# Kernel optimization log

Hardware: AMD Instinct MI355X
Metric: run time of the kernel (lower is better)

The kernel has to match this reference:

```python
import jax, jax.numpy as jnp
import numpy as np

NOISE_EPS = 0.01
TOP_K = 2


def setup_inputs() -> dict:
    key = jax.random.key(0)
    k1, k2, k3, k4 = jax.random.split(key, 4)
    B, S, D, E = 8, 4096, 1024, 16
    x = jax.random.normal(k1, (B, S, D), dtype=jnp.float32)
    noise = jax.random.normal(k2, (B * S, E), dtype=jnp.float32)
    # xavier_uniform for Linear(D, E): bound = sqrt(6/(D+E))
    bound = float(np.sqrt(6.0 / (D + E)))
    W_gate = jax.random.uniform(k3, (E, D), dtype=jnp.float32, minval=-bound, maxval=bound)
    W_noise = jax.random.uniform(k4, (E, D), dtype=jnp.float32, minval=-bound, maxval=bound)
    return {"x": x, "noise": noise, "W_gate": W_gate, "W_noise": W_noise}


def reference(x, noise, W_gate, W_noise):
    # flatten tokens: (B,S,D) -> (N,D)
    orig_shape = x.shape
    x_flat = x.reshape(-1, x.shape[-1])
    clean_logits = jnp.einsum('nd,ed->ne', x_flat, W_gate)          # (N, E)
    noise_logits = jnp.einsum('nd,ed->ne', x_flat, W_noise)         # (N, E)
    noisy_logits = clean_logits + noise * jax.nn.softplus(noise_logits) * NOISE_EPS
    gates = jax.nn.softmax(noisy_logits, axis=-1)                   # (N, E)
    top_k_gates, top_k_indices = jax.lax.top_k(gates, TOP_K)        # (N, k)
    top_k_gates = top_k_gates / (jnp.sum(top_k_gates, axis=-1, keepdims=True) + 1e-8)
    load = jnp.sum(gates, axis=0)                                    # (E,)
    new_shape = orig_shape[:-1] + (TOP_K,)
    top_k_gates = top_k_gates.reshape(new_shape)
    top_k_indices = top_k_indices.reshape(new_shape)
    return top_k_gates, top_k_indices, load
```

## Files before the change

kernel.cpp:

```cpp
#include <hip/hip_runtime.h>
#include <hip/hip_bf16.h>
#include <math.h>

#define N_TOK 32768
#define DDIM 1024
#define NEXP 16
#define THREADS 256
#define TOK_PER_WAVE 16
#define TOK_PER_BLK 64
#define NBLK (N_TOK / TOK_PER_BLK)
#define KSTEPS (DDIM / 32)

typedef __attribute__((ext_vector_type(8))) short bf16x8;
typedef __attribute__((ext_vector_type(4))) float f32x4;

__device__ inline short f2bf(float f) {
    __hip_bfloat16 h = __float2bfloat16(f);
    return __builtin_bit_cast(short, h);
}

__global__ __launch_bounds__(256) void make_wfrag(
    const float* __restrict__ Wg, const float* __restrict__ Wn,
    unsigned short* __restrict__ Wfrag)
{
    const int i    = blockIdx.x * 256 + threadIdx.x;
    const int j    = i & 7;
    const int lane = (i >> 3) & 63;
    const int tile = (i >> 9) & 1;
    const int s    = i >> 10;
    const int k    = s * 32 + (lane >> 4) * 8 + j;
    const float* W = tile ? Wn : Wg;
    Wfrag[i] = (unsigned short)f2bf(W[(size_t)(lane & 15) * DDIM + k]);
}

__global__ __launch_bounds__(THREADS) void router_mfma(
    const float* __restrict__ x, const float* __restrict__ noise,
    const unsigned short* __restrict__ Wfrag,
    float* __restrict__ out_gates, float* __restrict__ out_idx,
    float* __restrict__ partials)
{
    __shared__ float blk_load[NEXP];
    const int tid  = threadIdx.x;
    const int lane = tid & 63;
    const int w    = tid >> 6;
    if (tid < NEXP) blk_load[tid] = 0.0f;
    __syncthreads();

    const int tok = blockIdx.x * TOK_PER_BLK + w * TOK_PER_WAVE + (lane & 15);
    const int grp = lane >> 4;

    const float*          xb = x + (size_t)tok * DDIM + grp * 8;
    const unsigned short* wb = Wfrag + (size_t)lane * 8;

    f32x4 acc0 = {0.f, 0.f, 0.f, 0.f};
    f32x4 acc1 = {0.f, 0.f, 0.f, 0.f};

#pragma unroll 8
    for (int s = 0; s < KSTEPS; ++s) {
        const float4 lo = *(const float4*)(xb + s * 32);
        const float4 hi = *(const float4*)(xb + s * 32 + 4);
        const bf16x8 a0 = *(const bf16x8*)(wb + (size_t)(s * 2 + 0) * 512);
        const bf16x8 a1 = *(const bf16x8*)(wb + (size_t)(s * 2 + 1) * 512);
        bf16x8 b;
        b[0] = f2bf(lo.x); b[1] = f2bf(lo.y); b[2] = f2bf(lo.z); b[3] = f2bf(lo.w);
        b[4] = f2bf(hi.x); b[5] = f2bf(hi.y); b[6] = f2bf(hi.z); b[7] = f2bf(hi.w);
        acc0 = __builtin_amdgcn_mfma_f32_16x16x32_bf16(a0, b, acc0, 0, 0, 0);
        acc1 = __builtin_amdgcn_mfma_f32_16x16x32_bf16(a1, b, acc1, 0, 0, 0);
    }

    const float4 nz4 = *(const float4*)(noise + (size_t)tok * NEXP + grp * 4);
    const float nzv[4] = {nz4.x, nz4.y, nz4.z, nz4.w};

    float lg[4];
#pragma unroll
    for (int r = 0; r < 4; ++r) {
        const float cl = acc0[r];
        const float nl = acc1[r];
        const float sp = fmaxf(nl, 0.0f) + log1pf(expf(-fabsf(nl)));
        lg[r] = cl + nzv[r] * sp * 0.01f;
    }

    float m = fmaxf(fmaxf(lg[0], lg[1]), fmaxf(lg[2], lg[3]));
    m = fmaxf(m, __shfl_xor(m, 16, 64));
    m = fmaxf(m, __shfl_xor(m, 32, 64));

    float p[4];
    float ssum = 0.0f;
#pragma unroll
    for (int r = 0; r < 4; ++r) { p[r] = expf(lg[r] - m); ssum += p[r]; }
    ssum += __shfl_xor(ssum, 16, 64);
    ssum += __shfl_xor(ssum, 32, 64);
    const float inv = 1.0f / ssum;

    float g[4];
#pragma unroll
    for (int r = 0; r < 4; ++r) g[r] = p[r] * inv;

    float v1 = -1.0f, v2 = -1.0f;
    int   i1 = 0,     i2 = 0;
#pragma unroll
    for (int r = 0; r < 4; ++r) {
        const float ge = g[r];
        const int   e  = grp * 4 + r;
        if (ge > v1)      { v2 = v1; i2 = i1; v1 = ge; i1 = e; }
        else if (ge > v2) { v2 = ge; i2 = e; }
    }
#pragma unroll
    for (int off = 16; off <= 32; off <<= 1) {
        const float ov1 = __shfl_xor(v1, off, 64);
        const float ov2 = __shfl_xor(v2, off, 64);
        const int   oi1 = __shfl_xor(i1, off, 64);
        const int   oi2 = __shfl_xor(i2, off, 64);
        const bool aWins = (v1 > ov1) || (v1 == ov1 && i1 < oi1);
        float nv1, nv2; int ni1, ni2;
        if (aWins) {
            nv1 = v1; ni1 = i1;
            const bool bNext = (ov1 > v2) || (ov1 == v2 && oi1 < i2);
            nv2 = bNext ? ov1 : v2;  ni2 = bNext ? oi1 : i2;
        } else {
            nv1 = ov1; ni1 = oi1;
            const bool aNext = (v1 > ov2) || (v1 == ov2 && i1 < oi2);
            nv2 = aNext ? v1 : ov2;  ni2 = aNext ? i1 : oi2;
        }
        v1 = nv1; v2 = nv2; i1 = ni1; i2 = ni2;
    }
    if (grp == 0) {
        const float den = v1 + v2 + 1e-8f;
        out_gates[(size_t)tok * 2 + 0] = v1 / den;
        out_gates[(size_t)tok * 2 + 1] = v2 / den;
        out_idx[(size_t)tok * 2 + 0] = (float)i1;
        out_idx[(size_t)tok * 2 + 1] = (float)i2;
    }

#pragma unroll
    for (int r = 0; r < 4; ++r) {
        float v = g[r];
        v += __shfl_xor(v, 1, 64);
        v += __shfl_xor(v, 2, 64);
        v += __shfl_xor(v, 4, 64);
        v += __shfl_xor(v, 8, 64);
        if ((lane & 15) == 0) atomicAdd(&blk_load[grp * 4 + r], v);
    }
    __syncthreads();
    if (tid < NEXP) partials[(size_t)blockIdx.x * NEXP + tid] = blk_load[tid];
}

__global__ __launch_bounds__(64) void reduce_load(
    const float* __restrict__ partials, float* __restrict__ out_load)
{
    const int lane = threadIdx.x;
    float loc[16];
#pragma unroll
    for (int e = 0; e < 16; ++e) loc[e] = 0.0f;
    for (int b = lane; b < NBLK; b += 64) {
        const float4* p = (const float4*)(partials + (size_t)b * 16);
#pragma unroll
        for (int j = 0; j < 4; ++j) {
            const float4 v = p[j];
            loc[j * 4 + 0] += v.x; loc[j * 4 + 1] += v.y;
            loc[j * 4 + 2] += v.z; loc[j * 4 + 3] += v.w;
        }
    }
#pragma unroll
    for (int e = 0; e < 16; ++e) {
        float v = loc[e];
#pragma unroll
        for (int off = 32; off; off >>= 1) v += __shfl_xor(v, off, 64);
        if (lane == 0) out_load[e] = v;
    }
}

extern "C" void kernel_launch(void* const* d_in, const int* in_sizes, int n_in,
                              void* d_out, int out_size, void* d_ws, size_t ws_size,
                              hipStream_t stream) {
    (void)in_sizes; (void)n_in; (void)ws_size; (void)out_size;
    const float* x     = (const float*)d_in[0];
    const float* noise = (const float*)d_in[1];
    const float* Wg    = (const float*)d_in[2];
    const float* Wn    = (const float*)d_in[3];

    float* out       = (float*)d_out;
    float* out_gates = out;
    float* out_idx   = out + (size_t)N_TOK * 2;
    float* out_load  = out + (size_t)N_TOK * 4;

    unsigned short* Wfrag = (unsigned short*)d_ws;
    float* partials = (float*)((char*)d_ws + 65536);

    make_wfrag<<<128, 256, 0, stream>>>(Wg, Wn, Wfrag);
    router_mfma<<<NBLK, THREADS, 0, stream>>>(
        x, noise, Wfrag, out_gates, out_idx, partials);
    reduce_load<<<1, 64, 0, stream>>>(partials, out_load);
}
```

Before: 39.90 us.

## Stage x tiles into LDS via async global_load_lds with double buffering

The x tile for each block is now copied into LDS in 128-column chunks with the async global-to-LDS load instruction. Two swizzled buffers let the next chunk load while MFMAs run on the current one, and an XOR swizzle cuts bank conflicts on the LDS reads. This replaces per-lane strided global loads of x and aims to improve coalescing and hide memory latency. The cost is 64KB of LDS per block, which limits occupancy, plus one barrier per chunk.

```diff
diff --git a/kernel.cpp b/kernel.cpp
--- a/kernel.cpp
+++ b/kernel.cpp
@@ -9,7 +9,7 @@
 #define TOK_PER_WAVE 16
 #define TOK_PER_BLK 64
 #define NBLK (N_TOK / TOK_PER_BLK)
-#define KSTEPS (DDIM / 32)
+#define NCH 8
 
 typedef __attribute__((ext_vector_type(8))) short bf16x8;
 typedef __attribute__((ext_vector_type(4))) float f32x4;
@@ -39,33 +39,62 @@
     float* __restrict__ out_gates, float* __restrict__ out_idx,
     float* __restrict__ partials)
 {
+    __shared__ float xlds[2][8192];
     __shared__ float blk_load[NEXP];
+
     const int tid  = threadIdx.x;
     const int lane = tid & 63;
     const int w    = tid >> 6;
+    const int tokBase = blockIdx.x * TOK_PER_BLK;
     if (tid < NEXP) blk_load[tid] = 0.0f;
-    __syncthreads();
-
-    const int tok = blockIdx.x * TOK_PER_BLK + w * TOK_PER_WAVE + (lane & 15);
-    const int grp = lane >> 4;
-
-    const float*          xb = x + (size_t)tok * DDIM + grp * 8;
+
+    auto stage = [&](int buf, int c) {
+#pragma unroll
+        for (int it = 0; it < 8; ++it) {
+            const int slot = it * 256 + tid;
+            const int t    = slot >> 5;
+            const int q    = slot & 31;
+            const int pl   = ((q >> 1) ^ (t & 3)) * 2 + (q & 1);
+            const float* src = x + (size_t)(tokBase + t) * DDIM + c * 128 + pl * 4;
+            __builtin_amdgcn_global_load_lds(
+                (const __attribute__((address_space(1))) void*)src,
+                (__attribute__((address_space(3))) void*)
+                    ((char*)&xlds[buf][0] + (size_t)(it * 256 + w * 64) * 16),
+                16, 0, 0);
+        }
+    };
+
+    const int t_my = w * 16 + (lane & 15);
+    const int grp  = lane >> 4;
+    const int tok  = tokBase + t_my;
+
     const unsigned short* wb = Wfrag + (size_t)lane * 8;
 
     f32x4 acc0 = {0.f, 0.f, 0.f, 0.f};
     f32x4 acc1 = {0.f, 0.f, 0.f, 0.f};
 
-#pragma unroll 8
-    for (int s = 0; s < KSTEPS; ++s) {
-        const float4 lo = *(const float4*)(xb + s * 32);
-        const float4 hi = *(const float4*)(xb + s * 32 + 4);
-        const bf16x8 a0 = *(const bf16x8*)(wb + (size_t)(s * 2 + 0) * 512);
-        const bf16x8 a1 = *(const bf16x8*)(wb + (size_t)(s * 2 + 1) * 512);
-        bf16x8 b;
-        b[0] = f2bf(lo.x); b[1] = f2bf(lo.y); b[2] = f2bf(lo.z); b[3] = f2bf(lo.w);
-        b[4] = f2bf(hi.x); b[5] = f2bf(hi.y); b[6] = f2bf(hi.z); b[7] = f2bf(hi.w);
-        acc0 = __builtin_amdgcn_mfma_f32_16x16x32_bf16(a0, b, acc0, 0, 0, 0);
-        acc1 = __builtin_amdgcn_mfma_f32_16x16x32_bf16(a1, b, acc1, 0, 0, 0);
+    stage(0, 0);
+    __syncthreads();
+
+    for (int c = 0; c < NCH; ++c) {
+        if (c + 1 < NCH) stage((c + 1) & 1, c + 1);
+        const char* xb = (const char*)&xlds[c & 1][0];
+
+#pragma unroll
+        for (int s2 = 0; s2 < 4; ++s2) {
+            const int s    = c * 4 + s2;
+            const int phys = (s2 * 4 + grp) ^ (t_my & 3);
+            const float4 lo = *(const float4*)(xb + (size_t)t_my * 512 + phys * 32);
+            const float4 hi = *(const float4*)(xb + (size_t)t_my * 512 + phys * 32 + 16);
+            const bf16x8 a0 = *(const bf16x8*)(wb + (size_t)(s * 2 + 0) * 512);
+            const bf16x8 a1 = *(const bf16x8*)(wb + (size_t)(s * 2 + 1) * 512);
+            bf16x8 b;
+            b[0] = f2bf(lo.x); b[1] = f2bf(lo.y); b[2] = f2bf(lo.z); b[3] = f2bf(lo.w);
+            b[4] = f2bf(hi.x); b[5] = f2bf(hi.y); b[6] = f2bf(hi.z); b[7] = f2bf(hi.w);
+            acc0 = __builtin_amdgcn_mfma_f32_16x16x32_bf16(a0, b, acc0, 0, 0, 0);
+            acc1 = __builtin_amdgcn_mfma_f32_16x16x32_bf16(a1, b, acc1, 0, 0, 0);
+        }
+        __syncthreads();
     }
 
     const float4 nz4 = *(const float4*)(noise + (size_t)tok * NEXP + grp * 4);
```

After: 43.06 us. 1.08x slower.

## Fuse weight fragment packing into router kernel via per-block LDS staging

Applied to the files above, without the earlier changes.

Drops the separate weight-packing kernel. Each block now loads both fp32 weight matrices, converts them to bf16 in MFMA fragment order and stores them in 64 KB of shared memory, and the MMA loop reads fragments from LDS instead of global memory. This removes one kernel launch and the global round trip for the packed weights. In exchange, all 512 blocks repeat the 128 KB weight read and conversion, and the 64 KB LDS footprint caps occupancy at a few blocks per CU, which can hurt latency hiding for the streaming x loads.

```diff
diff --git a/kernel.cpp b/kernel.cpp
--- a/kernel.cpp
+++ b/kernel.cpp
@@ -19,38 +19,44 @@
     return __builtin_bit_cast(short, h);
 }
 
-__global__ __launch_bounds__(256) void make_wfrag(
-    const float* __restrict__ Wg, const float* __restrict__ Wn,
-    unsigned short* __restrict__ Wfrag)
-{
-    const int i    = blockIdx.x * 256 + threadIdx.x;
-    const int j    = i & 7;
-    const int lane = (i >> 3) & 63;
-    const int tile = (i >> 9) & 1;
-    const int s    = i >> 10;
-    const int k    = s * 32 + (lane >> 4) * 8 + j;
-    const float* W = tile ? Wn : Wg;
-    Wfrag[i] = (unsigned short)f2bf(W[(size_t)(lane & 15) * DDIM + k]);
-}
-
 __global__ __launch_bounds__(THREADS) void router_mfma(
     const float* __restrict__ x, const float* __restrict__ noise,
-    const unsigned short* __restrict__ Wfrag,
+    const float* __restrict__ Wg, const float* __restrict__ Wn,
     float* __restrict__ out_gates, float* __restrict__ out_idx,
     float* __restrict__ partials)
 {
+    __shared__ unsigned short wlds[32768];
     __shared__ float blk_load[NEXP];
+
     const int tid  = threadIdx.x;
     const int lane = tid & 63;
     const int w    = tid >> 6;
+
+#pragma unroll
+    for (int cc = 0; cc < 16; ++cc) {
+        const int slot  = cc * 256 + tid;
+        const int laneP = slot & 63;
+        const int tile  = (slot >> 6) & 1;
+        const int s     = slot >> 7;
+        const int m     = laneP & 15;
+        const int half  = laneP >> 4;
+        const int k0    = s * 32 + half * 8;
+        const float* Wsrc = (tile ? Wn : Wg) + (size_t)m * DDIM + k0;
+        const float4 f0 = *(const float4*)Wsrc;
+        const float4 f1 = *(const float4*)(Wsrc + 4);
+        bf16x8 v;
+        v[0] = f2bf(f0.x); v[1] = f2bf(f0.y); v[2] = f2bf(f0.z); v[3] = f2bf(f0.w);
+        v[4] = f2bf(f1.x); v[5] = f2bf(f1.y); v[6] = f2bf(f1.z); v[7] = f2bf(f1.w);
+        *(bf16x8*)&wlds[(size_t)slot * 8] = v;
+    }
     if (tid < NEXP) blk_load[tid] = 0.0f;
     __syncthreads();
 
     const int tok = blockIdx.x * TOK_PER_BLK + w * TOK_PER_WAVE + (lane & 15);
     const int grp = lane >> 4;
 
-    const float*          xb = x + (size_t)tok * DDIM + grp * 8;
-    const unsigned short* wb = Wfrag + (size_t)lane * 8;
+    const float* xb = x + (size_t)tok * DDIM + grp * 8;
+    const unsigned short* wb = &wlds[(size_t)lane * 8];
 
     f32x4 acc0 = {0.f, 0.f, 0.f, 0.f};
     f32x4 acc1 = {0.f, 0.f, 0.f, 0.f};
@@ -184,11 +190,9 @@
     float* out_idx   = out + (size_t)N_TOK * 2;
     float* out_load  = out + (size_t)N_TOK * 4;
 
-    unsigned short* Wfrag = (unsigned short*)d_ws;
-    float* partials = (float*)((char*)d_ws + 65536);
+    float* partials = (float*)d_ws;
 
-    make_wfrag<<<128, 256, 0, stream>>>(Wg, Wn, Wfrag);
     router_mfma<<<NBLK, THREADS, 0, stream>>>(
-        x, noise, Wfrag, out_gates, out_idx, partials);
+        x, noise, Wg, Wn, out_gates, out_idx, partials);
     reduce_load<<<1, 64, 0, stream>>>(partials, out_load);
 }
```

Measured after the change: 40.74 us. 2.1% more time.
